# Kernel optimization log

Measured on AMD Instinct MI355X. Metric: run time of the kernel, lower is better.

Reference implementation:

```python
import jax, jax.numpy as jnp
import numpy as np

B, L, E, H = 2, 2048, 2048, 16
HD = E // H  # 128


def build_rope(length, head_dim, base=10000.0):
    # [L, head_dim//2, 2] with [..., 0]=sin, [..., 1]=cos (matches apply_rope indexing)
    half = head_dim // 2
    inv_freq = 1.0 / (base ** (jnp.arange(half, dtype=jnp.float32) * 2.0 / head_dim))
    ang = jnp.arange(length, dtype=jnp.float32)[:, None] * inv_freq[None, :]  # [L, half]
    return jnp.stack([jnp.sin(ang), jnp.cos(ang)], axis=-1)  # [L, half, 2]


def apply_rope(x, rope):
    # x: [B, L, H, D]; rope: [L, D//2, 2] (sin, cos)
    b, l, h, d = x.shape
    sin = rope[:, :, 0].reshape(1, l, 1, d // 2)
    cos = rope[:, :, 1].reshape(1, l, 1, d // 2)
    xr = x.reshape(b, l, h, d // 2, 2)
    q0, q1 = xr[..., 0], xr[..., 1]
    out = jnp.stack([q0 * cos - q1 * sin, q1 * cos + q0 * sin], axis=-1)
    return out.reshape(b, l, h, d)


def setup_inputs() -> dict:
    key = jax.random.key(0)
    k1, k2, k3 = jax.random.split(key, 3)
    x = jax.random.normal(k1, (B, L, E), dtype=jnp.float32)
    w_attn = jax.random.normal(k2, (3 * E, E), dtype=jnp.float32) * (E ** -0.5)
    w_proj = jax.random.normal(k3, (E, E), dtype=jnp.float32) * (E ** -0.5)
    rope = build_rope(L, HD)
    return {"x": x, "rope": rope, "w_attn": w_attn, "w_proj": w_proj}


def reference(x, rope, w_attn, w_proj):
    b, l, e = x.shape
    h, hd = H, HD
    qkv = jnp.einsum('ble,fe->blf', x, w_attn)  # [B, L, 3E]
    q, k, v = jnp.split(qkv, 3, axis=-1)
    q = apply_rope(q.reshape(b, l, h, hd), rope)
    k = apply_rope(k.reshape(b, l, h, hd), rope)
    v = v.reshape(b, l, h, hd)
    # causal SDPA, scale 1/sqrt(head_dim)
    scale = 1.0 / np.sqrt(hd).astype(np.float32)
    scores = jnp.einsum('bqhd,bkhd->bhqk', q, k) * scale
    causal = jnp.tril(jnp.ones((l, l), dtype=bool))
    scores = jnp.where(causal[None, None], scores, jnp.finfo(scores.dtype).min)
    att = jax.nn.softmax(scores, axis=-1)
    y = jnp.einsum('bhqk,bkhd->bqhd', att, v).reshape(b, l, e)
    return jnp.einsum('ble,fe->blf', y, w_proj)
```

## Files before the change

### kernel.cpp

```cpp
#include <hip/hip_runtime.h>
#include <math.h>

#define BATCH 2
#define LSEQ  2048
#define EMB   2048
#define NH    16
#define HD    128

typedef __attribute__((ext_vector_type(8))) short bf16x8;
typedef __attribute__((ext_vector_type(8))) unsigned short u16x8;
typedef __attribute__((ext_vector_type(4))) float f32x4;

static __device__ __forceinline__ unsigned short f2bf(float f) {
    unsigned u = __float_as_uint(f);
    u += 0x7fffu + ((u >> 16) & 1u);
    return (unsigned short)(u >> 16);
}

static __device__ __forceinline__ void load_lds16(const void* g, void* l) {
    __builtin_amdgcn_global_load_lds(
        (const __attribute__((address_space(1))) void*)g,
        (__attribute__((address_space(3))) void*)l, 16, 0, 0);
}

#define N1 (BATCH * LSEQ * EMB)
#define N2 (3 * EMB * EMB)
#define N3 (EMB * EMB)

__global__ __launch_bounds__(256) void cast_bf16_kernel(
    const float* __restrict__ x, const float* __restrict__ wa,
    const float* __restrict__ wp,
    unsigned short* __restrict__ xb, unsigned short* __restrict__ wab,
    unsigned short* __restrict__ wpb)
{
    size_t i4 = ((size_t)blockIdx.x * 256 + threadIdx.x) * 4;
    const float* src;
    unsigned short* dst;
    size_t off;
    if (i4 < (size_t)N1) { src = x; dst = xb; off = i4; }
    else if (i4 < (size_t)N1 + N2) { src = wa; dst = wab; off = i4 - N1; }
    else { src = wp; dst = wpb; off = i4 - N1 - N2; }
    float4 f = *(const float4*)(src + off);
    ushort4 u;
    u.x = f2bf(f.x); u.y = f2bf(f.y); u.z = f2bf(f.z); u.w = f2bf(f.w);
    *(ushort4*)(dst + off) = u;
}

__global__ __launch_bounds__(256) void gemm_bt_bf16(
    const unsigned short* __restrict__ A, const unsigned short* __restrict__ B,
    const float* __restrict__ rope,
    float* __restrict__ C,
    unsigned short* __restrict__ qo, unsigned short* __restrict__ ko,
    unsigned short* __restrict__ vo,
    int M, int N, int K, int mode)
{
    __shared__ unsigned short As[128 * 64];
    __shared__ unsigned short Bs[128 * 64];

    const int tid = threadIdx.x;
    const int lane = tid & 63;
    const int w = tid >> 6;
    const int m = lane & 15;
    const int g = lane >> 4;
    const int wm = (w & 1) * 64;
    const int wn = (w >> 1) * 64;

    const int nwgx = gridDim.x;
    const int lin = blockIdx.y * nwgx + blockIdx.x;
    const int cpx = (nwgx * gridDim.y) >> 3;
    const int swz = (lin & 7) * cpx + (lin >> 3);
    const int bm = (swz / nwgx) * 128;
    const int bn = (swz % nwgx) * 128;

    f32x4 acc[4][4];
#pragma unroll
    for (int mi = 0; mi < 4; mi++)
#pragma unroll
        for (int ni = 0; ni < 4; ni++) acc[mi][ni] = (f32x4){0.f, 0.f, 0.f, 0.f};

    for (int k0 = 0; k0 < K; k0 += 64) {
        __syncthreads();
#pragma unroll
        for (int i = 0; i < 4; i++) {
            const int idx = i * 256 + tid;
            const int row = idx >> 3;
            const int c = (idx & 7) ^ (row & 7);
            load_lds16(A + (size_t)(bm + row) * K + k0 + c * 8, &As[idx * 8]);
            load_lds16(B + (size_t)(bn + row) * K + k0 + c * 8, &Bs[idx * 8]);
        }
        __syncthreads();

#pragma unroll
        for (int kc = 0; kc < 2; kc++) {
            bf16x8 af[4], bfv[4];
#pragma unroll
            for (int mi = 0; mi < 4; mi++) {
                const int row = wm + mi * 16 + m;
                af[mi] = *(const bf16x8*)&As[(row * 8 + ((kc * 4 + g) ^ (m & 7))) * 8];
            }
#pragma unroll
            for (int ni = 0; ni < 4; ni++) {
                const int row = wn + ni * 16 + m;
                bfv[ni] = *(const bf16x8*)&Bs[(row * 8 + ((kc * 4 + g) ^ (m & 7))) * 8];
            }
#pragma unroll
            for (int mi = 0; mi < 4; mi++)
#pragma unroll
                for (int ni = 0; ni < 4; ni++)
                    acc[mi][ni] = __builtin_amdgcn_mfma_f32_16x16x32_bf16(
                        af[mi], bfv[ni], acc[mi][ni], 0, 0, 0);
        }
    }

#pragma unroll
    for (int mi = 0; mi < 4; mi++) {
#pragma unroll
        for (int ni = 0; ni < 4; ni++) {
            const int col = bn + wn + ni * 16 + m;
            if (mode == 0) {
#pragma unroll
                for (int r = 0; r < 4; r++) {
                    const int row = bm + wm + mi * 16 + g * 4 + r;
                    C[(size_t)row * N + col] = acc[mi][ni][r];
                }
            } else {
                const int which = col >> 11;
                const int e = col & 2047;
                const int h = e >> 7;
                const int d = e & 127;
                if (which < 2) {
                    unsigned short* dst = (which == 0) ? qo : ko;
                    const int t2 = ((d >> 1) << 1);
#pragma unroll
                    for (int r = 0; r < 4; r++) {
                        const int row = bm + wm + mi * 16 + g * 4 + r;
                        const int b = row >> 11;
                        const int l = row & 2047;
                        float val = acc[mi][ni][r];
                        const float prt = __shfl_xor(val, 1);
                        const float2 sc = *(const float2*)(rope + (size_t)l * HD + t2);
                        val = (m & 1) ? fmaf(val, sc.y, prt * sc.x)
                                      : fmaf(val, sc.y, -prt * sc.x);
                        dst[(((size_t)(b * NH + h)) * LSEQ + l) * HD + d] = f2bf(val);
                    }
                } else {
                    const int l0 = bm + wm + mi * 16 + g * 4;
                    const int b = l0 >> 11;
                    const int l = l0 & 2047;
                    ushort4 vv;
                    vv.x = f2bf(acc[mi][ni][0]);
                    vv.y = f2bf(acc[mi][ni][1]);
                    vv.z = f2bf(acc[mi][ni][2]);
                    vv.w = f2bf(acc[mi][ni][3]);
                    *(ushort4*)(vo + (((size_t)(b * NH + h)) * HD + d) * LSEQ + l) = vv;
                }
            }
        }
    }
}

#define PTILES 32
#define PS_STR 68

__global__ __launch_bounds__(256) void attn_kernel(
    const unsigned short* __restrict__ q, const unsigned short* __restrict__ k,
    const unsigned short* __restrict__ vT, unsigned short* __restrict__ y)
{
    __shared__ __align__(16) unsigned short Ks[2][64 * 128];
    __shared__ __align__(16) unsigned short Vs[2][64 * 128];
    __shared__ __align__(16) unsigned short Ps[64 * PS_STR];

    const int tid = threadIdx.x;
    const int lane = tid & 63;
    const int w = tid >> 6;
    const int m = lane & 15;
    const int g = lane >> 4;
    const int bh = blockIdx.x;
    const int qt = PTILES - 1 - blockIdx.y;
    const int q0 = qt * 64;
    const size_t base = (size_t)bh * LSEQ * HD;
    const float scale = 0.08838834764831845f;
    const int bB = bh / NH;
    const int hh = bh % NH;
    const int sw = m & 7;

    auto stage = [&](int buf, int kb0) {
        const unsigned short* ksrc = k + base + (size_t)kb0 * HD;
#pragma unroll
        for (int i = 0; i < 4; i++) {
            const int idx = i * 256 + tid;
            const int row = idx >> 4;
            const int c = (idx & 15) ^ (row & 7);
            load_lds16(ksrc + (size_t)row * HD + c * 8, &Ks[buf][idx * 8]);
        }
#pragma unroll
        for (int i = 0; i < 4; i++) {
            const int idx = i * 256 + tid;
            const int d = idx >> 3;
            const int c = (idx & 7) ^ (d & 7);
            load_lds16(vT + base + (size_t)d * LSEQ + kb0 + c * 8, &Vs[buf][idx * 8]);
        }
    };

    bf16x8 aq[4];
    {
        const unsigned short* qrow = q + base + (size_t)(q0 + w * 16 + m) * HD;
#pragma unroll
        for (int kc = 0; kc < 4; kc++)
            aq[kc] = *(const bf16x8*)(qrow + kc * 32 + g * 8);
    }

    f32x4 o[8];
#pragma unroll
    for (int i = 0; i < 8; i++) o[i] = (f32x4){0.f, 0.f, 0.f, 0.f};
    float mprev[4], lsum[4];
#pragma unroll
    for (int r = 0; r < 4; r++) { mprev[r] = -1e30f; lsum[r] = 0.f; }

    stage(0, 0);
    int cur = 0;

    for (int kt = 0; kt <= qt; kt++) {
        const int k0 = kt * 64;

        __syncthreads();

        if (kt < qt) stage(cur ^ 1, k0 + 64);

        const unsigned short* Kc = Ks[cur];
        const unsigned short* Vc = Vs[cur];

        f32x4 s[4];
#pragma unroll
        for (int n = 0; n < 4; n++) {
            f32x4 acc = (f32x4){0.f, 0.f, 0.f, 0.f};
#pragma unroll
            for (int kc = 0; kc < 4; kc++) {
                const int row = n * 16 + m;
                bf16x8 bk = *(const bf16x8*)&Kc[(row * 16 + ((kc * 4 + g) ^ sw)) * 8];
                acc = __builtin_amdgcn_mfma_f32_16x16x32_bf16(aq[kc], bk, acc, 0, 0, 0);
            }
            s[n] = acc;
        }

        const int rowg = q0 + w * 16 + g * 4;
        if (kt == qt) {
#pragma unroll
            for (int n = 0; n < 4; n++) {
                const int col = k0 + n * 16 + m;
#pragma unroll
                for (int r = 0; r < 4; r++) {
                    const float val = s[n][r] * scale;
                    s[n][r] = (col <= rowg + r) ? val : -1e30f;
                }
            }
        } else {
#pragma unroll
            for (int n = 0; n < 4; n++)
#pragma unroll
                for (int r = 0; r < 4; r++) s[n][r] *= scale;
        }

        float al[4];
#pragma unroll
        for (int r = 0; r < 4; r++) {
            float v0 = fmaxf(fmaxf(s[0][r], s[1][r]), fmaxf(s[2][r], s[3][r]));
            v0 = fmaxf(v0, __shfl_xor(v0, 1));
            v0 = fmaxf(v0, __shfl_xor(v0, 2));
            v0 = fmaxf(v0, __shfl_xor(v0, 4));
            v0 = fmaxf(v0, __shfl_xor(v0, 8));
            const float mn = fmaxf(mprev[r], v0);
            al[r] = __expf(mprev[r] - mn);
            mprev[r] = mn;
        }
#pragma unroll
        for (int r = 0; r < 4; r++) {
            float sum = 0.f;
#pragma unroll
            for (int n = 0; n < 4; n++) {
                const float p = __expf(s[n][r] - mprev[r]);
                sum += p;
                Ps[(w * 16 + g * 4 + r) * PS_STR + n * 16 + m] = f2bf(p);
            }
            sum += __shfl_xor(sum, 1);
            sum += __shfl_xor(sum, 2);
            sum += __shfl_xor(sum, 4);
            sum += __shfl_xor(sum, 8);
            lsum[r] = lsum[r] * al[r] + sum;
        }

#pragma unroll
        for (int dc = 0; dc < 8; dc++)
#pragma unroll
            for (int r = 0; r < 4; r++) o[dc][r] *= al[r];

        bf16x8 ap[2];
#pragma unroll
        for (int kk = 0; kk < 2; kk++)
            ap[kk] = *(const bf16x8*)&Ps[(w * 16 + m) * PS_STR + kk * 32 + g * 8];
#pragma unroll
        for (int dc = 0; dc < 8; dc++) {
#pragma unroll
            for (int kk = 0; kk < 2; kk++) {
                const int row = dc * 16 + m;
                bf16x8 bv = *(const bf16x8*)&Vc[(row * 8 + ((kk * 4 + g) ^ sw)) * 8];
                o[dc] = __builtin_amdgcn_mfma_f32_16x16x32_bf16(ap[kk], bv, o[dc], 0, 0, 0);
            }
        }

        cur ^= 1;
    }

#pragma unroll
    for (int r = 0; r < 4; r++) {
        const float inv = 1.f / lsum[r];
        const int lrow = q0 + w * 16 + g * 4 + r;
        unsigned short* dst = y + (((size_t)bB * LSEQ + lrow) * NH + hh) * HD;
#pragma unroll
        for (int dc = 0; dc < 8; dc++)
            dst[dc * 16 + m] = f2bf(o[dc][r] * inv);
    }
}

extern "C" void kernel_launch(void* const* d_in, const int* in_sizes, int n_in,
                              void* d_out, int out_size, void* d_ws, size_t ws_size,
                              hipStream_t stream) {
    const float* x      = (const float*)d_in[0];
    const float* rope   = (const float*)d_in[1];
    const float* w_attn = (const float*)d_in[2];
    const float* w_proj = (const float*)d_in[3];
    float* out = (float*)d_out;
    unsigned short* ws = (unsigned short*)d_ws;

    const size_t per = (size_t)BATCH * NH * LSEQ * HD;
    unsigned short* qb  = ws;
    unsigned short* kb  = ws + per;
    unsigned short* vb  = ws + 2 * per;
    unsigned short* yb  = ws + 3 * per;
    unsigned short* xb  = ws + 4 * per;
    unsigned short* wab = xb + (size_t)N1;
    unsigned short* wpb = wab + (size_t)N2;

    const int M = BATCH * LSEQ;

    const int cast_blocks = (N1 + N2 + N3) / 4 / 256;
    cast_bf16_kernel<<<cast_blocks, 256, 0, stream>>>(x, w_attn, w_proj, xb, wab, wpb);

    dim3 g1(3 * EMB / 128, M / 128);
    gemm_bt_bf16<<<g1, 256, 0, stream>>>(xb, wab, rope, nullptr, qb, kb, vb,
                                         M, 3 * EMB, EMB, 1);

    dim3 ga(BATCH * NH, PTILES);
    attn_kernel<<<ga, 256, 0, stream>>>(qb, kb, vb, yb);

    dim3 g2(EMB / 128, M / 128);
    gemm_bt_bf16<<<g2, 256, 0, stream>>>(yb, wpb, nullptr, out,
                                         nullptr, nullptr, nullptr, M, EMB, EMB, 0);
}
```

Baseline: 407.1 us.

## Use 256x256 double-buffered GEMM tiles with 512 threads and MFMA priority

The bf16 GEMM moves from 128x128 tiles with 256 threads to 256x256 tiles with 8 waves. LDS is double-buffered so the async global-to-LDS loads for the next K step overlap the MFMAs on the current step, synchronised with explicit vmcnt waits. Each wave keeps its B fragments in registers across the M sub-tiles and raises its scheduling priority around the MFMA blocks. The aim is more operand reuse per LDS byte and hidden load latency. The cost is far fewer blocks (128 for the output projection), which can leave many CUs idle, plus a large LDS footprint and more accumulator registers.

```diff
diff --git a/kernel.cpp b/kernel.cpp
--- a/kernel.cpp
+++ b/kernel.cpp
@@ -46,7 +46,7 @@
     *(ushort4*)(dst + off) = u;
 }
 
-__global__ __launch_bounds__(256) void gemm_bt_bf16(
+__global__ __launch_bounds__(512, 2) void gemm_bt_bf16(
     const unsigned short* __restrict__ A, const unsigned short* __restrict__ B,
     const float* __restrict__ rope,
     float* __restrict__ C,
@@ -54,73 +54,101 @@
     unsigned short* __restrict__ vo,
     int M, int N, int K, int mode)
 {
-    __shared__ unsigned short As[128 * 64];
-    __shared__ unsigned short Bs[128 * 64];
+    __shared__ __align__(16) unsigned short As[2][256 * 64];
+    __shared__ __align__(16) unsigned short Bs[2][256 * 64];
 
     const int tid = threadIdx.x;
     const int lane = tid & 63;
     const int w = tid >> 6;
     const int m = lane & 15;
     const int g = lane >> 4;
-    const int wm = (w & 1) * 64;
-    const int wn = (w >> 1) * 64;
+    const int wr = w >> 2;
+    const int wc = w & 3;
+    const int sw = m & 7;
 
     const int nwgx = gridDim.x;
     const int lin = blockIdx.y * nwgx + blockIdx.x;
     const int cpx = (nwgx * gridDim.y) >> 3;
     const int swz = (lin & 7) * cpx + (lin >> 3);
-    const int bm = (swz / nwgx) * 128;
-    const int bn = (swz % nwgx) * 128;
-
-    f32x4 acc[4][4];
-#pragma unroll
-    for (int mi = 0; mi < 4; mi++)
-#pragma unroll
-        for (int ni = 0; ni < 4; ni++) acc[mi][ni] = (f32x4){0.f, 0.f, 0.f, 0.f};
-
-    for (int k0 = 0; k0 < K; k0 += 64) {
-        __syncthreads();
+    const int bm = (swz / nwgx) * 256;
+    const int bn = (swz % nwgx) * 256;
+
+    auto stage = [&](int buf, int k0) {
 #pragma unroll
         for (int i = 0; i < 4; i++) {
-            const int idx = i * 256 + tid;
+            const int idx = i * 512 + tid;
             const int row = idx >> 3;
             const int c = (idx & 7) ^ (row & 7);
-            load_lds16(A + (size_t)(bm + row) * K + k0 + c * 8, &As[idx * 8]);
-            load_lds16(B + (size_t)(bn + row) * K + k0 + c * 8, &Bs[idx * 8]);
-        }
-        __syncthreads();
-
-#pragma unroll
-        for (int kc = 0; kc < 2; kc++) {
-            bf16x8 af[4], bfv[4];
-#pragma unroll
-            for (int mi = 0; mi < 4; mi++) {
-                const int row = wm + mi * 16 + m;
-                af[mi] = *(const bf16x8*)&As[(row * 8 + ((kc * 4 + g) ^ (m & 7))) * 8];
-            }
-#pragma unroll
-            for (int ni = 0; ni < 4; ni++) {
-                const int row = wn + ni * 16 + m;
-                bfv[ni] = *(const bf16x8*)&Bs[(row * 8 + ((kc * 4 + g) ^ (m & 7))) * 8];
-            }
-#pragma unroll
-            for (int mi = 0; mi < 4; mi++)
+            load_lds16(A + (size_t)(bm + row) * K + k0 + c * 8, &As[buf][idx * 8]);
+            load_lds16(B + (size_t)(bn + row) * K + k0 + c * 8, &Bs[buf][idx * 8]);
+        }
+    };
+
+    f32x4 acc[8][4];
+#pragma unroll
+    for (int mi = 0; mi < 8; mi++)
+#pragma unroll
+        for (int ni = 0; ni < 4; ni++) acc[mi][ni] = (f32x4){0.f, 0.f, 0.f, 0.f};
+
+    const int nt = K >> 6;
+
+    stage(0, 0);
+
+    for (int t = 0; t < nt; t++) {
+        if (t + 1 < nt) {
+            stage((t + 1) & 1, (t + 1) * 64);
+            asm volatile("s_waitcnt vmcnt(8)" ::: "memory");
+        } else {
+            asm volatile("s_waitcnt vmcnt(0)" ::: "memory");
+        }
+        __builtin_amdgcn_s_barrier();
+
+        const unsigned short* Ac = As[t & 1];
+        const unsigned short* Bc = Bs[t & 1];
+
+        bf16x8 bfv[4][2];
+#pragma unroll
+        for (int ni = 0; ni < 4; ni++) {
+            const int row = wc * 64 + ni * 16 + m;
+#pragma unroll
+            for (int kc = 0; kc < 2; kc++)
+                bfv[ni][kc] = *(const bf16x8*)&Bc[(row * 8 + ((kc * 4 + g) ^ sw)) * 8];
+        }
+
+#pragma unroll
+        for (int p = 0; p < 4; p++) {
+            bf16x8 af[2][2];
+#pragma unroll
+            for (int mi2 = 0; mi2 < 2; mi2++) {
+                const int row = wr * 128 + (p * 2 + mi2) * 16 + m;
+#pragma unroll
+                for (int kc = 0; kc < 2; kc++)
+                    af[mi2][kc] = *(const bf16x8*)&Ac[(row * 8 + ((kc * 4 + g) ^ sw)) * 8];
+            }
+            __builtin_amdgcn_s_setprio(1);
+#pragma unroll
+            for (int mi2 = 0; mi2 < 2; mi2++)
 #pragma unroll
                 for (int ni = 0; ni < 4; ni++)
-                    acc[mi][ni] = __builtin_amdgcn_mfma_f32_16x16x32_bf16(
-                        af[mi], bfv[ni], acc[mi][ni], 0, 0, 0);
-        }
-    }
-
-#pragma unroll
-    for (int mi = 0; mi < 4; mi++) {
+#pragma unroll
+                    for (int kc = 0; kc < 2; kc++)
+                        acc[p * 2 + mi2][ni] = __builtin_amdgcn_mfma_f32_16x16x32_bf16(
+                            af[mi2][kc], bfv[ni][kc], acc[p * 2 + mi2][ni], 0, 0, 0);
+            __builtin_amdgcn_s_setprio(0);
+        }
+
+        __builtin_amdgcn_s_barrier();
+    }
+
+#pragma unroll
+    for (int mi = 0; mi < 8; mi++) {
 #pragma unroll
         for (int ni = 0; ni < 4; ni++) {
-            const int col = bn + wn + ni * 16 + m;
+            const int col = bn + wc * 64 + ni * 16 + m;
             if (mode == 0) {
 #pragma unroll
                 for (int r = 0; r < 4; r++) {
-                    const int row = bm + wm + mi * 16 + g * 4 + r;
+                    const int row = bm + wr * 128 + mi * 16 + g * 4 + r;
                     C[(size_t)row * N + col] = acc[mi][ni][r];
                 }
             } else {
@@ -133,7 +161,7 @@
                     const int t2 = ((d >> 1) << 1);
 #pragma unroll
                     for (int r = 0; r < 4; r++) {
-                        const int row = bm + wm + mi * 16 + g * 4 + r;
+                        const int row = bm + wr * 128 + mi * 16 + g * 4 + r;
                         const int b = row >> 11;
                         const int l = row & 2047;
                         float val = acc[mi][ni][r];
@@ -144,7 +172,7 @@
                         dst[(((size_t)(b * NH + h)) * LSEQ + l) * HD + d] = f2bf(val);
                     }
                 } else {
-                    const int l0 = bm + wm + mi * 16 + g * 4;
+                    const int l0 = bm + wr * 128 + mi * 16 + g * 4;
                     const int b = l0 >> 11;
                     const int l = l0 & 2047;
                     ushort4 vv;
@@ -346,14 +374,14 @@
     const int cast_blocks = (N1 + N2 + N3) / 4 / 256;
     cast_bf16_kernel<<<cast_blocks, 256, 0, stream>>>(x, w_attn, w_proj, xb, wab, wpb);
 
-    dim3 g1(3 * EMB / 128, M / 128);
-    gemm_bt_bf16<<<g1, 256, 0, stream>>>(xb, wab, rope, nullptr, qb, kb, vb,
+    dim3 g1(3 * EMB / 256, M / 256);
+    gemm_bt_bf16<<<g1, 512, 0, stream>>>(xb, wab, rope, nullptr, qb, kb, vb,
                                          M, 3 * EMB, EMB, 1);
 
     dim3 ga(BATCH * NH, PTILES);
     attn_kernel<<<ga, 256, 0, stream>>>(qb, kb, vb, yb);
 
-    dim3 g2(EMB / 128, M / 128);
-    gemm_bt_bf16<<<g2, 256, 0, stream>>>(yb, wpb, nullptr, out,
+    dim3 g2(EMB / 256, M / 256);
+    gemm_bt_bf16<<<g2, 512, 0, stream>>>(yb, wpb, nullptr, out,
                                          nullptr, nullptr, nullptr, M, EMB, EMB, 0);
 }
```

New measurement: 433.9 us. 1.07x slower.
